# Performance work log

Measured on AMD Instinct MI355X. Metric: run time of the kernel, lower is better.

## Reference

```python
import jax, jax.numpy as jnp
import numpy as np

N = 8192
D = 1024
TIME_DECAY = 86400.0
EPS = 1e-10


def setup_inputs() -> dict:
    key = jax.random.key(0)
    ks = jax.random.split(key, 8)
    x = jax.random.normal(ks[0], (N, D), dtype=jnp.float32)
    # timestamps spanning ~10 days so decay bias is non-trivial
    timestamps = jax.random.uniform(ks[1], (N,), dtype=jnp.float32) * (10.0 * TIME_DECAY)
    s = 1.0 / np.sqrt(D)
    Wq = jax.random.normal(ks[2], (D, D), dtype=jnp.float32) * s
    bq = jnp.zeros((D,), dtype=jnp.float32)
    Wk = jax.random.normal(ks[3], (D, D), dtype=jnp.float32) * s
    bk = jnp.zeros((D,), dtype=jnp.float32)
    Wv = jax.random.normal(ks[4], (D, D), dtype=jnp.float32) * s
    bv = jnp.zeros((D,), dtype=jnp.float32)
    return {"x": x, "timestamps": timestamps, "Wq": Wq, "bq": bq,
            "Wk": Wk, "bk": bk, "Wv": Wv, "bv": bv}


def reference(x, timestamps, Wq, bq, Wk, bk, Wv, bv):
    scale = jnp.asarray(D ** 0.5, x.dtype)
    # torch nn.Linear: y = x @ W.T + b
    Q = x @ Wq.T + bq          # [N, D]
    K = x @ Wk.T + bk          # [N, D]
    V = x @ Wv.T + bv          # [N, D]
    time_diff = timestamps[:, None] - timestamps[None, :]   # [N, N]
    time_decay = jnp.exp(-jnp.abs(time_diff) / TIME_DECAY)  # [N, N]
    scores = (Q @ K.T) / scale + jnp.log(time_decay + EPS)  # [N, N]
    attn = jax.nn.softmax(scores, axis=-1)
    return attn @ V
```

## Files before the change

kernel.cpp:

```cpp
#include <hip/hip_runtime.h>


using half8   = __attribute__((ext_vector_type(8))) _Float16;
using half4   = __attribute__((ext_vector_type(4))) _Float16;
using floatx4 = __attribute__((ext_vector_type(4))) float;

__device__ __forceinline__ void gload_lds16(const void* g, void* l) {
  __builtin_amdgcn_global_load_lds((const __attribute__((address_space(1))) void*)g,
                                   (__attribute__((address_space(3))) void*)l,
                                   16, 0, 0);
}

template<int N> __device__ __forceinline__ void waitv() {
  if constexpr (N == 12)     asm volatile("s_waitcnt vmcnt(12)" ::: "memory");
  else if constexpr (N == 8) asm volatile("s_waitcnt vmcnt(8)"  ::: "memory");
  else if constexpr (N == 6) asm volatile("s_waitcnt vmcnt(6)"  ::: "memory");
  else                       asm volatile("s_waitcnt vmcnt(0)"  ::: "memory");
}

template<int BM, int BN, int WM, int WN, int SLOTS, int MI, int NJ>
__device__ __forceinline__ void kloop64(
    const _Float16* __restrict__ A, const _Float16* __restrict__ B,
    long rowBase, long colBase, int lda, int ldb, int K,
    _Float16* __restrict__ As, _Float16* __restrict__ Bs,
    floatx4 (&acc)[MI][NJ])
{
  static_assert(MI == BM / WM / 16 && NJ == BN / WN / 16);
  constexpr int LA = BM / 64, LB = BN / 64;
  constexpr int ISS = LA + LB;
  const int tid = threadIdx.x;
  const int w = tid >> 6, lane = tid & 63;
  const int q = lane >> 4, l15 = lane & 15;
  const int wr = w / WN, wcn = w & (WN - 1);

  const int sc = ((lane & 7) ^ (lane >> 3)) << 3;
  const _Float16* Agp[LA]; const _Float16* Bgp[LB];
#pragma unroll
  for (int p = 0; p < LA; ++p)
    Agp[p] = A + (rowBase + p * 64 + (tid >> 3)) * (long)lda + sc;
#pragma unroll
  for (int p = 0; p < LB; ++p)
    Bgp[p] = B + (colBase + p * 64 + (tid >> 3)) * (long)ldb + sc;
  const int ldsOff = tid * 8;

  const int aRow = wr * (BM / WM) + l15;
  const int bRow = wcn * (BN / WN) + l15;
  const int cx = l15 & 7;

  auto issue = [&](int t, int slot) {
    const int ko = t << 6;
    _Float16* Asl = As + slot * (BM * 64);
    _Float16* Bsl = Bs + slot * (BN * 64);
#pragma unroll
    for (int p = 0; p < LA; ++p) gload_lds16(Agp[p] + ko, Asl + p * 4096 + ldsOff);
#pragma unroll
    for (int p = 0; p < LB; ++p) gload_lds16(Bgp[p] + ko, Bsl + p * 4096 + ldsOff);
  };

  auto compute = [&](int slot) {
    const _Float16* Asl = As + slot * (BM * 64);
    const _Float16* Bsl = Bs + slot * (BN * 64);
#pragma unroll
    for (int kk = 0; kk < 2; ++kk) {
      const int pc = ((kk * 4 + q) ^ cx) << 3;
      half8 bfr[NJ];
#pragma unroll
      for (int j = 0; j < NJ; ++j)
        bfr[j] = *(const half8*)&Bsl[(bRow + 16 * j) * 64 + pc];
      half8 afr[MI];
#pragma unroll
      for (int i = 0; i < MI; ++i)
        afr[i] = *(const half8*)&Asl[(aRow + 16 * i) * 64 + pc];
      __builtin_amdgcn_s_setprio(1);
#pragma unroll
      for (int i = 0; i < MI; ++i)
#pragma unroll
        for (int j = 0; j < NJ; ++j)
          acc[i][j] = __builtin_amdgcn_mfma_f32_16x16x32_f16(afr[i], bfr[j], acc[i][j], 0, 0, 0);
      __builtin_amdgcn_s_setprio(0);
    }
  };

  const int NT = K >> 6;
  if constexpr (SLOTS == 2) {
    issue(0, 0);
    int cs = 0;
    for (int t = 0; t < NT - 1; ++t) {
      issue(t + 1, cs ^ 1);
      waitv<ISS>();
      __builtin_amdgcn_s_barrier();
      compute(cs);
      __builtin_amdgcn_s_barrier();
      cs ^= 1;
    }
    waitv<0>(); __builtin_amdgcn_s_barrier();
    compute(cs);
  } else {
    static_assert(SLOTS == 3);
    issue(0, 0); issue(1, 1);
    int cs = 0, is = 2;
    for (int t = 0; t < NT - 2; ++t) {
      issue(t + 2, is);
      waitv<2 * ISS>();
      __builtin_amdgcn_s_barrier();
      compute(cs);
      __builtin_amdgcn_s_barrier();
      cs = (cs == 2) ? 0 : cs + 1;
      is = (is == 2) ? 0 : is + 1;
    }
    waitv<ISS>(); __builtin_amdgcn_s_barrier();
    compute(cs);  __builtin_amdgcn_s_barrier();
    cs = (cs == 2) ? 0 : cs + 1;
    waitv<0>();   __builtin_amdgcn_s_barrier();
    compute(cs);
  }
}

template<int BM, int BN, int WM, int WN, int SLOTS, int BIAS_MODE, int OUT_MODE, int SWZ>
__global__ __launch_bounds__(512, 2)
void gemm256_k(const _Float16* __restrict__ A, const _Float16* __restrict__ B,
               void* __restrict__ Cout, const float* __restrict__ bias,
               int lda, int ldb, int ldc, int K, float outScale)
{
  constexpr int MI = BM / WM / 16, NJ = BN / WN / 16;
  __shared__ __align__(16) _Float16 As[SLOTS * BM * 64];
  __shared__ __align__(16) _Float16 Bs[SLOTS * BN * 64];

  int tx, ty;
  if (SWZ) {
    const int bflat = blockIdx.y * gridDim.x + blockIdx.x;
    ty = bflat % gridDim.y;
    tx = bflat / gridDim.y;
  } else {
    tx = blockIdx.x; ty = blockIdx.y;
  }
  const long rowBase = (long)ty * BM;
  const long colBase = (long)tx * BN;

  floatx4 acc[MI][NJ] = {};
  kloop64<BM, BN, WM, WN, SLOTS, MI, NJ>(A, B, rowBase, colBase, lda, ldb, K, As, Bs, acc);

  const int tid = threadIdx.x;
  const int w = tid >> 6, lane = tid & 63;
  const int q = lane >> 4, l15 = lane & 15;
  const int wr = w / WN, wcn = w & (WN - 1);
#pragma unroll
  for (int i = 0; i < MI; ++i) {
#pragma unroll
    for (int r = 0; r < 4; ++r) {
      const long rowg = rowBase + wr * (BM / WM) + 16 * i + q * 4 + r;
#pragma unroll
      for (int j = 0; j < NJ; ++j) {
        const long colg = colBase + wcn * (BN / WN) + 16 * j + l15;
        float v = acc[i][j][r];
        if (BIAS_MODE == 1) v += bias[colg];
        if (BIAS_MODE == 2) v += bias[rowg];
        if (BIAS_MODE == 3) v *= bias[rowg];
        v *= outScale;
        if (OUT_MODE == 2) ((float*)Cout)[rowg * ldc + colg] = v;
        else               ((_Float16*)Cout)[rowg * ldc + colg] = (_Float16)v;
      }
    }
  }
}

__global__ __launch_bounds__(512, 2)
void gemm_stats256_k(const _Float16* __restrict__ A, const _Float16* __restrict__ B,
                     const float* __restrict__ ts, _Float16* __restrict__ U,
                     float* __restrict__ part, int lda, int ldb, int N, int K,
                     float qkScale)
{
  constexpr int BM = 256, BN = 256, WM = 2, WN = 4, MI = 8, NJ = 4;
  __shared__ __align__(16) _Float16 As[2 * BM * 64];
  __shared__ __align__(16) _Float16 Bs[2 * BN * 64];
  __shared__ float trs[256], tcs[256];
  __shared__ float sL[2][4][128];
  const int tid = threadIdx.x;
  const long rowBase = (long)blockIdx.y * 256;
  const long colBase = (long)blockIdx.x * 256;

  if (tid < 256) {
    trs[tid] = ts[rowBase + tid];
    tcs[tid] = ts[colBase + tid];
  }

  floatx4 acc[MI][NJ] = {};
  kloop64<BM, BN, WM, WN, 2, MI, NJ>(A, B, rowBase, colBase, lda, ldb, K, As, Bs, acc);

  const int w = tid >> 6, lane = tid & 63;
  const int q = lane >> 4, l15 = lane & 15;
  const int wr = w >> 2, wcn = w & 3;
  const float inv_td = 1.0f / 86400.0f;
#pragma unroll
  for (int i = 0; i < 8; ++i) {
#pragma unroll
    for (int r = 0; r < 4; ++r) {
      const int rowl = wr * 128 + 16 * i + q * 4 + r;
      const float tr = trs[rowl];
      float ls = 0.0f;
#pragma unroll
      for (int j = 0; j < 4; ++j) {
        const int coll = wcn * 64 + 16 * j + l15;
        const float sv = acc[i][j][r] * qkScale
                       - fabsf(tr - tcs[coll]) * inv_td - 4.0f;
        const float u = __expf(sv);
        ls += u;
        U[(rowBase + rowl) * (long)N + (colBase + coll)] = (_Float16)u;
      }
      for (int mask = 1; mask <= 8; mask <<= 1)
        ls += __shfl_xor(ls, mask, 64);
      if (l15 == 0) sL[wr][wcn][16 * i + 4 * q + r] = ls;
    }
  }
  __syncthreads();
  if (tid < 256) {
    const int wr2 = tid >> 7, rl = tid & 127;
    part[(rowBase + tid) * 32 + blockIdx.x] =
        sL[wr2][0][rl] + sL[wr2][1][rl] + sL[wr2][2][rl] + sL[wr2][3][rl];
  }
}

__global__ void combine_k(const float* __restrict__ part, float* __restrict__ invL) {
  const int r = blockIdx.x * 256 + threadIdx.x;
  float L = 0.0f;
  for (int c = 0; c < 32; ++c) L += part[(long)r * 32 + c];
  invL[r] = 1.0f / L;
}

__global__ void cvt_k(const float* __restrict__ in, _Float16* __restrict__ out, int n) {
  const int i = (blockIdx.x * 256 + threadIdx.x) * 4;
  if (i >= n) return;
  const float4 v = *(const float4*)(in + i);
  half4 o = { (_Float16)v.x, (_Float16)v.y, (_Float16)v.z, (_Float16)v.w };
  *(half4*)(out + i) = o;
}

extern "C" void kernel_launch(void* const* d_in, const int* in_sizes, int n_in,
                              void* d_out, int out_size, void* d_ws, size_t ws_size,
                              hipStream_t stream)
{
  (void)in_sizes; (void)n_in; (void)out_size; (void)ws_size;
  const int N = 8192, D = 1024;
  const float* x  = (const float*)d_in[0];
  const float* ts = (const float*)d_in[1];
  const float* Wq = (const float*)d_in[2];
  const float* bq = (const float*)d_in[3];
  const float* Wk = (const float*)d_in[4];
  const float* bk = (const float*)d_in[5];
  const float* Wv = (const float*)d_in[6];
  const float* bv = (const float*)d_in[7];

  char* p = (char*)d_ws;
  auto grab = [&](size_t bytes) {
    char* r = p;
    p += (bytes + 255) & ~(size_t)255;
    return r;
  };
  _Float16* xh    = (_Float16*)grab((size_t)N * D * 2);
  _Float16* wqkh  = (_Float16*)grab((size_t)2 * D * D * 2);
  _Float16* wvh   = (_Float16*)grab((size_t)D * D * 2);
  _Float16* QKcat = (_Float16*)grab((size_t)N * 2 * D * 2);
  _Float16* VTh   = (_Float16*)grab((size_t)D * N * 2);
  _Float16* Uh    = (_Float16*)grab((size_t)N * N * 2);
  float*    part  = (float*)grab((size_t)N * 32 * sizeof(float));
  float*    invL  = (float*)grab((size_t)N * sizeof(float));
  float*    bcat  = (float*)grab((size_t)2 * D * sizeof(float));

  cvt_k<<<N * D / 1024, 256, 0, stream>>>(x,  xh,  N * D);
  cvt_k<<<D * D / 1024, 256, 0, stream>>>(Wq, wqkh,         D * D);
  cvt_k<<<D * D / 1024, 256, 0, stream>>>(Wk, wqkh + D * D, D * D);
  cvt_k<<<D * D / 1024, 256, 0, stream>>>(Wv, wvh, D * D);
  hipMemcpyAsync(bcat,     bq, D * sizeof(float), hipMemcpyDeviceToDevice, stream);
  hipMemcpyAsync(bcat + D, bk, D * sizeof(float), hipMemcpyDeviceToDevice, stream);

  dim3 blk(512);
  gemm256_k<256, 256, 2, 4, 2, 1, 0, 0><<<dim3(2 * D / 256, N / 256), blk, 0, stream>>>(
      xh, wqkh, QKcat, bcat, D, D, 2 * D, D, 1.0f);
  gemm256_k<256, 128, 4, 2, 3, 2, 0, 0><<<dim3(N / 128, D / 256), blk, 0, stream>>>(
      wvh, xh, VTh, bv, D, D, N, D, 1.0f);
  gemm_stats256_k<<<dim3(N / 256, N / 256), blk, 0, stream>>>(
      QKcat, QKcat + D, ts, Uh, part, 2 * D, 2 * D, N, D, 1.0f / 32.0f);
  combine_k<<<N / 256, 256, 0, stream>>>(part, invL);
  gemm256_k<256, 128, 4, 2, 3, 3, 2, 1><<<dim3(D / 128, N / 256), blk, 0, stream>>>(
      Uh, VTh, d_out, invL, N, N, D, N, 1.0f);
}
```

Measured before the change: 494.0 us.

## Split GEMM k-tile into phases interleaving LDS reads, staged loads and MFMAs

Restructures the shared GEMM main loop into per-phase chunks. Each phase reads a slice of A fragments (B fragments once per tile), issues part of the next tile's global-to-LDS loads, synchronises, then runs that slice's MFMAs. The goal is to spread memory issue across the compute and hide LDS-read latency behind matrix work, in the style of a ping-pong schedule. In exchange it adds more barriers per tile and changes the vmcnt waits, which could cost throughput or risk ordering mistakes.

```diff
diff --git a/kernel.cpp b/kernel.cpp
--- a/kernel.cpp
+++ b/kernel.cpp
@@ -12,22 +12,20 @@
 }
 
 template<int N> __device__ __forceinline__ void waitv() {
-  if constexpr (N == 12)     asm volatile("s_waitcnt vmcnt(12)" ::: "memory");
-  else if constexpr (N == 8) asm volatile("s_waitcnt vmcnt(8)"  ::: "memory");
-  else if constexpr (N == 6) asm volatile("s_waitcnt vmcnt(6)"  ::: "memory");
-  else                       asm volatile("s_waitcnt vmcnt(0)"  ::: "memory");
-}
-
-template<int BM, int BN, int WM, int WN, int SLOTS, int MI, int NJ>
-__device__ __forceinline__ void kloop64(
+  if constexpr (N == 6) asm volatile("s_waitcnt vmcnt(6)" ::: "memory");
+  else                  asm volatile("s_waitcnt vmcnt(0)" ::: "memory");
+}
+
+template<int BM, int BN, int WM, int WN, int SLOTS, int PH, int MI, int NJ>
+__device__ __forceinline__ void kloop_f(
     const _Float16* __restrict__ A, const _Float16* __restrict__ B,
     long rowBase, long colBase, int lda, int ldb, int K,
     _Float16* __restrict__ As, _Float16* __restrict__ Bs,
     floatx4 (&acc)[MI][NJ])
 {
-  static_assert(MI == BM / WM / 16 && NJ == BN / WN / 16);
+  static_assert(MI == BM / WM / 16 && NJ == BN / WN / 16 && MI % PH == 0);
   constexpr int LA = BM / 64, LB = BN / 64;
-  constexpr int ISS = LA + LB;
+  constexpr int RP = MI / PH;
   const int tid = threadIdx.x;
   const int w = tid >> 6, lane = tid & 63;
   const int q = lane >> 4, l15 = lane & 15;
@@ -47,76 +45,97 @@
   const int bRow = wcn * (BN / WN) + l15;
   const int cx = l15 & 7;
 
-  auto issue = [&](int t, int slot) {
+  auto issueA = [&](int t, int s) {
+    _Float16* Asl = As + s * (BM * 64);
     const int ko = t << 6;
-    _Float16* Asl = As + slot * (BM * 64);
-    _Float16* Bsl = Bs + slot * (BN * 64);
 #pragma unroll
     for (int p = 0; p < LA; ++p) gload_lds16(Agp[p] + ko, Asl + p * 4096 + ldsOff);
+  };
+  auto issueB = [&](int t, int s) {
+    _Float16* Bsl = Bs + s * (BN * 64);
+    const int ko = t << 6;
 #pragma unroll
     for (int p = 0; p < LB; ++p) gload_lds16(Bgp[p] + ko, Bsl + p * 4096 + ldsOff);
   };
 
-  auto compute = [&](int slot) {
+  half8 bfr[2][NJ];
+
+  auto tile = [&](int t, int slot, bool doStage, int ew) {
     const _Float16* Asl = As + slot * (BM * 64);
     const _Float16* Bsl = Bs + slot * (BN * 64);
-#pragma unroll
-    for (int kk = 0; kk < 2; ++kk) {
-      const int pc = ((kk * 4 + q) ^ cx) << 3;
-      half8 bfr[NJ];
-#pragma unroll
-      for (int j = 0; j < NJ; ++j)
-        bfr[j] = *(const half8*)&Bsl[(bRow + 16 * j) * 64 + pc];
-      half8 afr[MI];
-#pragma unroll
-      for (int i = 0; i < MI; ++i)
-        afr[i] = *(const half8*)&Asl[(aRow + 16 * i) * 64 + pc];
+    const int st = t + SLOTS - 1;
+    const int ss = (SLOTS == 2) ? (slot ^ 1) : (st % 3);
+#pragma unroll
+    for (int ph = 0; ph < PH; ++ph) {
+      half8 afr[2][RP];
+      if (ph == 0) {
+#pragma unroll
+        for (int kk = 0; kk < 2; ++kk) {
+          const int pc = ((kk * 4 + q) ^ cx) << 3;
+#pragma unroll
+          for (int j = 0; j < NJ; ++j)
+            bfr[kk][j] = *(const half8*)&Bsl[(bRow + 16 * j) * 64 + pc];
+        }
+      }
+#pragma unroll
+      for (int kk = 0; kk < 2; ++kk) {
+        const int pc = ((kk * 4 + q) ^ cx) << 3;
+#pragma unroll
+        for (int r = 0; r < RP; ++r)
+          afr[kk][r] = *(const half8*)&Asl[(aRow + 16 * (ph * RP + r)) * 64 + pc];
+      }
+      if (doStage && ph == 0) issueA(st, ss);
+      if (doStage && ph == 1) issueB(st, ss);
+      __builtin_amdgcn_s_barrier();
+      asm volatile("s_waitcnt lgkmcnt(0)" ::: "memory");
+      __builtin_amdgcn_sched_barrier(0);
       __builtin_amdgcn_s_setprio(1);
 #pragma unroll
-      for (int i = 0; i < MI; ++i)
-#pragma unroll
-        for (int j = 0; j < NJ; ++j)
-          acc[i][j] = __builtin_amdgcn_mfma_f32_16x16x32_f16(afr[i], bfr[j], acc[i][j], 0, 0, 0);
+      for (int kk = 0; kk < 2; ++kk)
+#pragma unroll
+        for (int r = 0; r < RP; ++r)
+#pragma unroll
+          for (int j = 0; j < NJ; ++j)
+            acc[ph * RP + r][j] = __builtin_amdgcn_mfma_f32_16x16x32_f16(
+                afr[kk][r], bfr[kk][j], acc[ph * RP + r][j], 0, 0, 0);
       __builtin_amdgcn_s_setprio(0);
+      if (ph == PH - 1) {
+        if (ew == 6)      waitv<6>();
+        else if (ew == 0) waitv<0>();
+        if (ew >= 0) __builtin_amdgcn_s_barrier();
+      } else {
+        __builtin_amdgcn_s_barrier();
+      }
     }
   };
 
   const int NT = K >> 6;
   if constexpr (SLOTS == 2) {
-    issue(0, 0);
+    issueA(0, 0); issueB(0, 0);
+    waitv<0>(); __builtin_amdgcn_s_barrier();
     int cs = 0;
     for (int t = 0; t < NT - 1; ++t) {
-      issue(t + 1, cs ^ 1);
-      waitv<ISS>();
-      __builtin_amdgcn_s_barrier();
-      compute(cs);
-      __builtin_amdgcn_s_barrier();
+      tile(t, cs, true, 0);
       cs ^= 1;
     }
-    waitv<0>(); __builtin_amdgcn_s_barrier();
-    compute(cs);
+    tile(NT - 1, cs, false, -1);
   } else {
     static_assert(SLOTS == 3);
-    issue(0, 0); issue(1, 1);
-    int cs = 0, is = 2;
-    for (int t = 0; t < NT - 2; ++t) {
-      issue(t + 2, is);
-      waitv<2 * ISS>();
-      __builtin_amdgcn_s_barrier();
-      compute(cs);
-      __builtin_amdgcn_s_barrier();
+    issueA(0, 0); issueB(0, 0);
+    issueA(1, 1); issueB(1, 1);
+    waitv<6>(); __builtin_amdgcn_s_barrier();
+    int cs = 0;
+    for (int t = 0; t < NT - 1; ++t) {
+      const bool st = (t + 2 < NT);
+      tile(t, cs, st, (t < NT - 2) ? 6 : 0);
       cs = (cs == 2) ? 0 : cs + 1;
-      is = (is == 2) ? 0 : is + 1;
-    }
-    waitv<ISS>(); __builtin_amdgcn_s_barrier();
-    compute(cs);  __builtin_amdgcn_s_barrier();
-    cs = (cs == 2) ? 0 : cs + 1;
-    waitv<0>();   __builtin_amdgcn_s_barrier();
-    compute(cs);
-  }
-}
-
-template<int BM, int BN, int WM, int WN, int SLOTS, int BIAS_MODE, int OUT_MODE, int SWZ>
+    }
+    tile(NT - 1, cs, false, -1);
+  }
+}
+
+template<int BM, int BN, int WM, int WN, int SLOTS, int PH,
+         int BIAS_MODE, int OUT_MODE, int SWZ>
 __global__ __launch_bounds__(512, 2)
 void gemm256_k(const _Float16* __restrict__ A, const _Float16* __restrict__ B,
                void* __restrict__ Cout, const float* __restrict__ bias,
@@ -138,7 +157,8 @@
   const long colBase = (long)tx * BN;
 
   floatx4 acc[MI][NJ] = {};
-  kloop64<BM, BN, WM, WN, SLOTS, MI, NJ>(A, B, rowBase, colBase, lda, ldb, K, As, Bs, acc);
+  kloop_f<BM, BN, WM, WN, SLOTS, PH, MI, NJ>(A, B, rowBase, colBase, lda, ldb, K,
+                                             As, Bs, acc);
 
   const int tid = threadIdx.x;
   const int w = tid >> 6, lane = tid & 63;
@@ -185,7 +205,8 @@
   }
 
   floatx4 acc[MI][NJ] = {};
-  kloop64<BM, BN, WM, WN, 2, MI, NJ>(A, B, rowBase, colBase, lda, ldb, K, As, Bs, acc);
+  kloop_f<BM, BN, WM, WN, 2, 4, MI, NJ>(A, B, rowBase, colBase, lda, ldb, K,
+                                        As, Bs, acc);
 
   const int w = tid >> 6, lane = tid & 63;
   const int q = lane >> 4, l15 = lane & 15;
@@ -274,13 +295,13 @@
   hipMemcpyAsync(bcat + D, bk, D * sizeof(float), hipMemcpyDeviceToDevice, stream);
 
   dim3 blk(512);
-  gemm256_k<256, 256, 2, 4, 2, 1, 0, 0><<<dim3(2 * D / 256, N / 256), blk, 0, stream>>>(
+  gemm256_k<256, 256, 2, 4, 2, 4, 1, 0, 0><<<dim3(2 * D / 256, N / 256), blk, 0, stream>>>(
       xh, wqkh, QKcat, bcat, D, D, 2 * D, D, 1.0f);
-  gemm256_k<256, 128, 4, 2, 3, 2, 0, 0><<<dim3(N / 128, D / 256), blk, 0, stream>>>(
+  gemm256_k<256, 128, 4, 2, 3, 2, 2, 0, 0><<<dim3(N / 128, D / 256), blk, 0, stream>>>(
       wvh, xh, VTh, bv, D, D, N, D, 1.0f);
   gemm_stats256_k<<<dim3(N / 256, N / 256), blk, 0, stream>>>(
       QKcat, QKcat + D, ts, Uh, part, 2 * D, 2 * D, N, D, 1.0f / 32.0f);
   combine_k<<<N / 256, 256, 0, stream>>>(part, invL);
-  gemm256_k<256, 128, 4, 2, 3, 3, 2, 1><<<dim3(D / 128, N / 256), blk, 0, stream>>>(
+  gemm256_k<256, 128, 4, 2, 3, 2, 3, 2, 1><<<dim3(D / 128, N / 256), blk, 0, stream>>>(
       Uh, VTh, d_out, invL, N, N, D, N, 1.0f);
 }
```

New measurement: 487.0 us. No clear change (-1.4%).
